# Kernel optimization log

Hardware: AMD Instinct MI355X
Metric: run time of the kernel (lower is better)

Reference implementation:

```python
import jax, jax.numpy as jnp
import numpy as np

B, D, L = 32, 64, 8192
K = 512
COMMITMENT_COST = 0.1


def setup_inputs() -> dict:
    key = jax.random.key(0)
    k1, k2 = jax.random.split(key)
    x = jax.random.normal(k1, (B, D, L), dtype=jnp.float32)
    # Embedding initialized uniform(-1/K, 1/K) as in the torch module
    weight = jax.random.uniform(k2, (K, D), dtype=jnp.float32, minval=-1.0 / K, maxval=1.0 / K)
    return {"x": x, "weight": weight}


def reference(x, weight):
    # x: [B, D, L] -> inputs: [B, L, D]
    inputs = jnp.transpose(x, (0, 2, 1))
    flat = inputs.reshape(-1, D)  # [N, D]
    # Squared L2 distances to codebook: [N, K]
    distances = (
        jnp.sum(flat * flat, axis=1, keepdims=True)
        + jnp.sum(weight * weight, axis=1)
        - 2.0 * flat @ weight.T
    )
    encoding_indices = jnp.argmin(distances, axis=1)  # [N]
    # Gather quantized vectors (equivalent to one-hot @ weight)
    quantized = weight[encoding_indices].reshape(inputs.shape)  # [B, L, D]
    e_latent_loss = jnp.mean((jax.lax.stop_gradient(quantized) - inputs) ** 2)
    q_latent_loss = jnp.mean((quantized - jax.lax.stop_gradient(inputs)) ** 2)
    loss = q_latent_loss + COMMITMENT_COST * e_latent_loss
    # Straight-through estimator
    quantized_st = inputs + jax.lax.stop_gradient(quantized - inputs)
    out = jnp.transpose(quantized_st, (0, 2, 1))  # [B, D, L]
    # perplexity = number of unique codes used (jit-friendly via bincount)
    perplexity = jnp.sum(jnp.bincount(encoding_indices, length=K) > 0)
    return (out, loss, perplexity, weight, encoding_indices[:, None])
```

## Files before the change

kernel.cpp:

```cpp
#include <hip/hip_runtime.h>
#include <math.h>

#define BB 32
#define DD 64
#define LL 8192
#define KK 512
#define NN (BB*LL)

#define OUT0_SZ  (BB*DD*LL)
#define LOSS_OFF (OUT0_SZ)
#define PERP_OFF (OUT0_SZ + 1)
#define W_OFF    (OUT0_SZ + 2)
#define IDX_OFF  (W_OFF + KK*DD)

#define WS_TVEC 0
#define WS_HIST 512
#define WS_LACC 1024
#define WS_WPH  1032
#define WS_WPL  (1032 + 16384)

typedef __attribute__((ext_vector_type(4))) float f32x4;
typedef __attribute__((ext_vector_type(8))) short s16x8;

#define WINDOW 1e-4f

__device__ __forceinline__ unsigned short f2bf(float f) {
  unsigned int u = __float_as_uint(f);
  return (unsigned short)((u + 0x7FFFu + ((u >> 16) & 1u)) >> 16);
}
__device__ __forceinline__ float bf2f(unsigned short s) {
  return __uint_as_float(((unsigned int)s) << 16);
}

__global__ void vq_init(const float* __restrict__ w, float* __restrict__ ws) {
#pragma clang fp contract(off)
  int t = blockIdx.x * blockDim.x + threadIdx.x;
  if (t < KK) {
    const float* wr = w + t * DD;
    float r[8];
#pragma unroll
    for (int j = 0; j < 8; j++) { float v = wr[j]; r[j] = v * v; }
#pragma unroll
    for (int blk = 8; blk < 64; blk += 8) {
#pragma unroll
      for (int j = 0; j < 8; j++) { float v = wr[blk + j]; float a = v * v; r[j] = r[j] + a; }
    }
    ws[WS_TVEC + t] = ((r[0] + r[1]) + (r[2] + r[3])) + ((r[4] + r[5]) + (r[6] + r[7]));
    ((int*)ws)[WS_HIST + t] = 0;
  }
  if (t == 0) ws[WS_LACC] = 0.0f;

  int j    = t & 7;
  int lane = (t >> 3) & 63;
  int ks   = (t >> 9) & 1;
  int ct   = t >> 10;
  int code = ct * 16 + (lane & 15);
  int d    = ks * 32 + ((lane >> 4) << 3) + j;
  float v  = w[code * DD + d];
  unsigned short h = f2bf(v);
  unsigned short l = f2bf(v - bf2f(h));
  ((unsigned short*)(ws + WS_WPH))[((ct * 2 + ks) * 64 + lane) * 8 + j] = h;
  ((unsigned short*)(ws + WS_WPL))[((ct * 2 + ks) * 64 + lane) * 8 + j] = l;
}

__launch_bounds__(256, 2)
__global__ void vq_main(const float* __restrict__ x, const float* __restrict__ w,
                        const float* __restrict__ ws, float* __restrict__ dout) {
#pragma clang fp contract(off)
  __shared__ unsigned short xstage[256 * 64];
  __shared__ float t_lds[KK];
  __shared__ float s_lds[256];
  __shared__ int   ccnt[256];
  __shared__ unsigned short cand[256][8];
  __shared__ unsigned char flags[KK];

  const float* tvec = ws + WS_TVEC;
  const s16x8* wph8 = (const s16x8*)(ws + WS_WPH);
  const s16x8* wpl8 = (const s16x8*)(ws + WS_WPL);
  int* hist = (int*)ws + WS_HIST;
  float* lacc = (float*)ws + WS_LACC;

  const int tid  = threadIdx.x;
  const int lane = tid & 63;
  const int wv   = tid >> 6;

  for (int e = tid; e < KK; e += 256) { t_lds[e] = tvec[e]; flags[e] = 0; }
  ccnt[tid] = 0;

  const int n = blockIdx.x * 256 + tid;
  const int b = n >> 13, l = n & 8191;
  const float* px = x + (size_t)b * DD * LL + l;

  float xr[64];
#pragma unroll
  for (int i = 0; i < 64; i++) xr[i] = px[(size_t)i * LL];

  float s;
  {
    float r[8];
#pragma unroll
    for (int j = 0; j < 8; j++) r[j] = xr[j] * xr[j];
#pragma unroll
    for (int blk = 8; blk < 64; blk += 8) {
#pragma unroll
      for (int j = 0; j < 8; j++) { float a = xr[blk + j] * xr[blk + j]; r[j] = r[j] + a; }
    }
    s = ((r[0] + r[1]) + (r[2] + r[3])) + ((r[4] + r[5]) + (r[6] + r[7]));
  }
  s_lds[tid] = s;

  {
    unsigned int* xs32 = (unsigned int*)xstage;
#pragma unroll
    for (int j = 0; j < 32; j++) {
      unsigned int v = (unsigned int)f2bf(xr[2 * j]) | ((unsigned int)f2bf(xr[2 * j + 1]) << 16);
      xs32[tid * 32 + j] = v;
    }
  }
  __syncthreads();

  s16x8 afh[4][2], afl[4][2];
  {
    const s16x8* xs8 = (const s16x8*)xstage;
#pragma unroll
    for (int tl = 0; tl < 4; tl++)
#pragma unroll
      for (int ks = 0; ks < 2; ks++)
        afh[tl][ks] = xs8[(wv * 64 + tl * 16 + (lane & 15)) * 8 + ks * 4 + (lane >> 4)];
  }
  __syncthreads();

  {
    unsigned int* xs32 = (unsigned int*)xstage;
#pragma unroll
    for (int j = 0; j < 32; j++) {
      float v0 = xr[2 * j],     h0 = bf2f(f2bf(v0));
      float v1 = xr[2 * j + 1], h1 = bf2f(f2bf(v1));
      unsigned int v = (unsigned int)f2bf(v0 - h0) | ((unsigned int)f2bf(v1 - h1) << 16);
      xs32[tid * 32 + j] = v;
    }
  }
  __syncthreads();
  {
    const s16x8* xs8 = (const s16x8*)xstage;
#pragma unroll
    for (int tl = 0; tl < 4; tl++)
#pragma unroll
      for (int ks = 0; ks < 2; ks++)
        afl[tl][ks] = xs8[(wv * 64 + tl * 16 + (lane & 15)) * 8 + ks * 4 + (lane >> 4)];
  }

  float sfr[4][4];
#pragma unroll
  for (int tl = 0; tl < 4; tl++)
#pragma unroll
    for (int r = 0; r < 4; r++)
      sfr[tl][r] = s_lds[wv * 64 + tl * 16 + ((lane >> 4) << 2) + r];

  unsigned long long t1[4][4], t2[4][4];
#pragma unroll
  for (int tl = 0; tl < 4; tl++)
#pragma unroll
    for (int r = 0; r < 4; r++) { t1[tl][r] = ~0ULL; t2[tl][r] = ~0ULL; }

#pragma clang loop unroll(disable)
  for (int ct = 0; ct < 32; ct++) {
    s16x8 bh0 = wph8[(ct * 2 + 0) * 64 + lane];
    s16x8 bh1 = wph8[(ct * 2 + 1) * 64 + lane];
    s16x8 bl0 = wpl8[(ct * 2 + 0) * 64 + lane];
    s16x8 bl1 = wpl8[(ct * 2 + 1) * 64 + lane];
    float tc = t_lds[ct * 16 + (lane & 15)];
    unsigned long long klo = (unsigned long long)(ct * 16 + (lane & 15));

#pragma unroll
    for (int tl = 0; tl < 4; tl++) {
      f32x4 acc = {0.f, 0.f, 0.f, 0.f};
      acc = __builtin_amdgcn_mfma_f32_16x16x32_bf16(afl[tl][0], bh0, acc, 0, 0, 0);
      acc = __builtin_amdgcn_mfma_f32_16x16x32_bf16(afl[tl][1], bh1, acc, 0, 0, 0);
      acc = __builtin_amdgcn_mfma_f32_16x16x32_bf16(afh[tl][0], bl0, acc, 0, 0, 0);
      acc = __builtin_amdgcn_mfma_f32_16x16x32_bf16(afh[tl][1], bl1, acc, 0, 0, 0);
      acc = __builtin_amdgcn_mfma_f32_16x16x32_bf16(afh[tl][0], bh0, acc, 0, 0, 0);
      acc = __builtin_amdgcn_mfma_f32_16x16x32_bf16(afh[tl][1], bh1, acc, 0, 0, 0);
#pragma unroll
      for (int r = 0; r < 4; r++) {
        float dap = fmaf(-2.0f, acc[r], sfr[tl][r] + tc);
        unsigned long long pk = (((unsigned long long)__float_as_uint(dap)) << 32) | klo;
        bool c1 = pk < t1[tl][r];
        bool c2 = pk < t2[tl][r];
        t2[tl][r] = c1 ? t1[tl][r] : (c2 ? pk : t2[tl][r]);
        t1[tl][r] = c1 ? pk : t1[tl][r];
      }
    }
  }

  unsigned long long g[4][4];
#pragma unroll
  for (int tl = 0; tl < 4; tl++)
#pragma unroll
    for (int r = 0; r < 4; r++) g[tl][r] = t1[tl][r];
#pragma unroll
  for (int m = 1; m <= 8; m <<= 1) {
#pragma unroll
    for (int tl = 0; tl < 4; tl++)
#pragma unroll
      for (int r = 0; r < 4; r++) {
        unsigned long long q = __shfl_xor(g[tl][r], m);
        g[tl][r] = q < g[tl][r] ? q : g[tl][r];
      }
  }

#pragma unroll
  for (int tl = 0; tl < 4; tl++)
#pragma unroll
    for (int r = 0; r < 4; r++) {
      int row = wv * 64 + tl * 16 + ((lane >> 4) << 2) + r;
      float thr = __uint_as_float((unsigned int)(g[tl][r] >> 32)) + WINDOW;
      float m1 = __uint_as_float((unsigned int)(t1[tl][r] >> 32));
      float m2 = __uint_as_float((unsigned int)(t2[tl][r] >> 32));
      bool in1 = (m1 <= thr), in2 = (m2 <= thr);
      if (in1) { int p = atomicAdd(&ccnt[row], 1); if (p < 8) cand[row][p] = (unsigned short)(t1[tl][r] & 0xFFFFu); }
      if (in2) { int p = atomicAdd(&ccnt[row], 1); if (p < 8) cand[row][p] = (unsigned short)(t2[tl][r] & 0xFFFFu); }
      if (in1 && in2) { int p = atomicAdd(&ccnt[row], 1); if (p < 8) cand[row][p] = (unsigned short)(512 + (lane & 15)); }
    }
  __syncthreads();

  int kwin;
  {
    int cnt = ccnt[tid];
    if (cnt == 1) {
      kwin = cand[tid][0];
    } else {
      unsigned long long best = ~0ULL;
      auto evalExact = [&](int c) {
        const float4* wr = (const float4*)(w + c * DD);
        float gg = 0.0f;
#pragma unroll
        for (int i = 0; i < 16; i++) {
          float4 wq = wr[i];
          gg = fmaf(xr[4 * i + 0], wq.x, gg); gg = fmaf(xr[4 * i + 1], wq.y, gg);
          gg = fmaf(xr[4 * i + 2], wq.z, gg); gg = fmaf(xr[4 * i + 3], wq.w, gg);
        }
        float de = fmaf(-2.0f, gg, s + t_lds[c]);
        unsigned long long pk = (((unsigned long long)__float_as_uint(de)) << 32) | (unsigned long long)c;
        if (pk < best) best = pk;
      };
      if (cnt > 8) {
        for (int c = 0; c < KK; c++) evalExact(c);
      } else {
        for (int i = 0; i < cnt; i++) {
          int c = cand[tid][i];
          if (c < 512) evalExact(c);
          else { int c0 = c - 512; for (int jj = 0; jj < 32; jj++) evalExact(jj * 16 + c0); }
        }
      }
      kwin = (int)(best & 0xFFFFu);
    }
  }

  float ls = 0.0f;
  {
    float* o = dout + (size_t)b * DD * LL + l;
    const float4* wr = (const float4*)(w + kwin * DD);
#pragma unroll
    for (int i = 0; i < 16; i++) {
      float4 v = wr[i];
      o[(size_t)(4 * i + 0) * LL] = v.x; o[(size_t)(4 * i + 1) * LL] = v.y;
      o[(size_t)(4 * i + 2) * LL] = v.z; o[(size_t)(4 * i + 3) * LL] = v.w;
      float df;
      df = v.x - xr[4 * i + 0]; ls = fmaf(df, df, ls);
      df = v.y - xr[4 * i + 1]; ls = fmaf(df, df, ls);
      df = v.z - xr[4 * i + 2]; ls = fmaf(df, df, ls);
      df = v.w - xr[4 * i + 3]; ls = fmaf(df, df, ls);
    }
  }
  dout[IDX_OFF + n] = (float)kwin;

#pragma unroll
  for (int o = 32; o > 0; o >>= 1) ls += __shfl_down(ls, o);
  if ((tid & 63) == 0) atomicAdd(lacc, ls);

  flags[kwin] = 1;
  __syncthreads();
  for (int e = tid; e < KK; e += 256)
    if (flags[e]) atomicOr(&hist[e], 1);
}

__global__ void vq_final(const float* __restrict__ w, const float* __restrict__ ws,
                         float* __restrict__ dout) {
  __shared__ int red[512];
  const int* hist = (const int*)ws + WS_HIST;
  int tid = threadIdx.x;
  red[tid] = (hist[tid] != 0) ? 1 : 0;
  __syncthreads();
  for (int sx = 256; sx > 0; sx >>= 1) {
    if (tid < sx) red[tid] += red[tid + sx];
    __syncthreads();
  }
  if (tid == 0) {
    dout[PERP_OFF] = (float)red[0];
    float m = ws[WS_LACC] / 16777216.0f;
    dout[LOSS_OFF] = m + 0.1f * m;
  }
  const float2* w2 = (const float2*)w;
  float2* o2 = (float2*)(dout + W_OFF);
  for (int j = tid; j < KK * DD / 2; j += 512) o2[j] = w2[j];
}

extern "C" void kernel_launch(void* const* d_in, const int* in_sizes, int n_in,
                              void* d_out, int out_size, void* d_ws, size_t ws_size,
                              hipStream_t stream) {
  const float* x = (const float*)d_in[0];
  const float* w = (const float*)d_in[1];
  float* dout = (float*)d_out;
  float* ws = (float*)d_ws;

  vq_init<<<128, 256, 0, stream>>>(w, ws);
  vq_main<<<NN / 256, 256, 0, stream>>>(x, w, ws, dout);
  vq_final<<<1, 512, 0, stream>>>(w, ws, dout);
}
```

Before: 246.0 us.

## Split each row across two lanes, swizzle LDS staging, prefetch codebook tiles

Each input row is now handled by two lanes, each loading half of the 64 features. This halves register pressure and doubles the grid size, at the cost of more MFMA passes per codebook tile relative to rows. The LDS staging for the bf16 hi/lo split uses XOR swizzling to avoid bank conflicts. Codebook fragments for the next tile are prefetched in the loop, and the top-2 tracking uses float plus a tile index instead of packed 64-bit keys. The weight copy moves from the single-block final kernel into the init kernel. The exact re-check now reloads the upper half of x from global memory and keeps only 4 candidate slots.

```diff
diff --git a/kernel.cpp b/kernel.cpp
--- a/kernel.cpp
+++ b/kernel.cpp
@@ -21,6 +21,7 @@
 
 typedef __attribute__((ext_vector_type(4))) float f32x4;
 typedef __attribute__((ext_vector_type(8))) short s16x8;
+typedef unsigned long long u64;
 
 #define WINDOW 1e-4f
 
@@ -31,8 +32,14 @@
 __device__ __forceinline__ float bf2f(unsigned short s) {
   return __uint_as_float(((unsigned int)s) << 16);
 }
-
-__global__ void vq_init(const float* __restrict__ w, float* __restrict__ ws) {
+__device__ __forceinline__ u64 shflx64(u64 v, int m) {
+  unsigned lo = __shfl_xor((unsigned)v, m);
+  unsigned hi = __shfl_xor((unsigned)(v >> 32), m);
+  return ((u64)hi << 32) | lo;
+}
+
+__global__ void vq_init(const float* __restrict__ w, float* __restrict__ ws,
+                        float* __restrict__ dout) {
 #pragma clang fp contract(off)
   int t = blockIdx.x * blockDim.x + threadIdx.x;
   if (t < KK) {
@@ -50,28 +57,35 @@
   }
   if (t == 0) ws[WS_LACC] = 0.0f;
 
-  int j    = t & 7;
-  int lane = (t >> 3) & 63;
-  int ks   = (t >> 9) & 1;
-  int ct   = t >> 10;
-  int code = ct * 16 + (lane & 15);
-  int d    = ks * 32 + ((lane >> 4) << 3) + j;
-  float v  = w[code * DD + d];
-  unsigned short h = f2bf(v);
-  unsigned short l = f2bf(v - bf2f(h));
-  ((unsigned short*)(ws + WS_WPH))[((ct * 2 + ks) * 64 + lane) * 8 + j] = h;
-  ((unsigned short*)(ws + WS_WPL))[((ct * 2 + ks) * 64 + lane) * 8 + j] = l;
+  {
+    int j    = t & 7;
+    int lane = (t >> 3) & 63;
+    int ks   = (t >> 9) & 1;
+    int ct   = t >> 10;
+    int code = ct * 16 + (lane & 15);
+    int d    = ks * 32 + ((lane >> 4) << 3) + j;
+    float v  = w[code * DD + d];
+    unsigned short h = f2bf(v);
+    unsigned short l = f2bf(v - bf2f(h));
+    ((unsigned short*)(ws + WS_WPH))[((ct * 2 + ks) * 64 + lane) * 8 + j] = h;
+    ((unsigned short*)(ws + WS_WPL))[((ct * 2 + ks) * 64 + lane) * 8 + j] = l;
+  }
+
+  if (t < KK * DD / 2) {
+    ((float2*)(dout + W_OFF))[t] = ((const float2*)w)[t];
+  }
 }
 
 __launch_bounds__(256, 2)
 __global__ void vq_main(const float* __restrict__ x, const float* __restrict__ w,
                         const float* __restrict__ ws, float* __restrict__ dout) {
 #pragma clang fp contract(off)
-  __shared__ unsigned short xstage[256 * 64];
+  __shared__ uint4 xstage[4][32][8];
   __shared__ float t_lds[KK];
-  __shared__ float s_lds[256];
-  __shared__ int   ccnt[256];
-  __shared__ unsigned short cand[256][8];
+  __shared__ float s_lds[128];
+  __shared__ u64   g_lds[128];
+  __shared__ unsigned short cand[128][4];
+  __shared__ int   ccnt[128];
   __shared__ unsigned char flags[KK];
 
   const float* tvec = ws + WS_TVEC;
@@ -83,210 +97,249 @@
   const int tid  = threadIdx.x;
   const int lane = tid & 63;
   const int wv   = tid >> 6;
+  const int rloc = lane & 31;
+  const int half = lane >> 5;
+  const int res  = lane & 15;
 
   for (int e = tid; e < KK; e += 256) { t_lds[e] = tvec[e]; flags[e] = 0; }
-  ccnt[tid] = 0;
-
-  const int n = blockIdx.x * 256 + tid;
+  if (tid < 128) ccnt[tid] = 0;
+
+  const int n = blockIdx.x * 128 + wv * 32 + rloc;
   const int b = n >> 13, l = n & 8191;
   const float* px = x + (size_t)b * DD * LL + l;
 
-  float xr[64];
-#pragma unroll
-  for (int i = 0; i < 64; i++) xr[i] = px[(size_t)i * LL];
-
-  float s;
+  float xh[32];
+#pragma unroll
+  for (int i = 0; i < 32; i++) xh[i] = px[(size_t)(half * 32 + i) * LL];
+
+  float s_apx;
   {
     float r[8];
 #pragma unroll
-    for (int j = 0; j < 8; j++) r[j] = xr[j] * xr[j];
-#pragma unroll
-    for (int blk = 8; blk < 64; blk += 8) {
-#pragma unroll
-      for (int j = 0; j < 8; j++) { float a = xr[blk + j] * xr[blk + j]; r[j] = r[j] + a; }
-    }
-    s = ((r[0] + r[1]) + (r[2] + r[3])) + ((r[4] + r[5]) + (r[6] + r[7]));
-  }
-  s_lds[tid] = s;
-
+    for (int j = 0; j < 8; j++) r[j] = xh[j] * xh[j];
+#pragma unroll
+    for (int blk = 8; blk < 32; blk += 8) {
+#pragma unroll
+      for (int j = 0; j < 8; j++) { float a = xh[blk + j] * xh[blk + j]; r[j] = r[j] + a; }
+    }
+    float sh = ((r[0] + r[1]) + (r[2] + r[3])) + ((r[4] + r[5]) + (r[6] + r[7]));
+    float so = __shfl(sh, lane ^ 32);
+    float slo = half ? so : sh, shi = half ? sh : so;
+    s_apx = slo + shi;
+    if (half == 0) s_lds[wv * 32 + rloc] = s_apx;
+  }
+
+  uint4* xs4 = (uint4*)xstage;
+  const s16x8* xs8 = (const s16x8*)xstage;
+  s16x8 afh[2][2], afl[2][2];
   {
-    unsigned int* xs32 = (unsigned int*)xstage;
-#pragma unroll
-    for (int j = 0; j < 32; j++) {
-      unsigned int v = (unsigned int)f2bf(xr[2 * j]) | ((unsigned int)f2bf(xr[2 * j + 1]) << 16);
-      xs32[tid * 32 + j] = v;
-    }
-  }
-  __syncthreads();
-
-  s16x8 afh[4][2], afl[4][2];
-  {
-    const s16x8* xs8 = (const s16x8*)xstage;
-#pragma unroll
-    for (int tl = 0; tl < 4; tl++)
-#pragma unroll
-      for (int ks = 0; ks < 2; ks++)
-        afh[tl][ks] = xs8[(wv * 64 + tl * 16 + (lane & 15)) * 8 + ks * 4 + (lane >> 4)];
-  }
-  __syncthreads();
-
-  {
-    unsigned int* xs32 = (unsigned int*)xstage;
-#pragma unroll
-    for (int j = 0; j < 32; j++) {
-      float v0 = xr[2 * j],     h0 = bf2f(f2bf(v0));
-      float v1 = xr[2 * j + 1], h1 = bf2f(f2bf(v1));
-      unsigned int v = (unsigned int)f2bf(v0 - h0) | ((unsigned int)f2bf(v1 - h1) << 16);
-      xs32[tid * 32 + j] = v;
-    }
-  }
-  __syncthreads();
-  {
-    const s16x8* xs8 = (const s16x8*)xstage;
-#pragma unroll
-    for (int tl = 0; tl < 4; tl++)
-#pragma unroll
-      for (int ks = 0; ks < 2; ks++)
-        afl[tl][ks] = xs8[(wv * 64 + tl * 16 + (lane & 15)) * 8 + ks * 4 + (lane >> 4)];
-  }
-
-  float sfr[4][4];
-#pragma unroll
-  for (int tl = 0; tl < 4; tl++)
+    unsigned int pk[16];
+#pragma unroll
+    for (int m = 0; m < 16; m++)
+      pk[m] = (unsigned int)f2bf(xh[2 * m]) | ((unsigned int)f2bf(xh[2 * m + 1]) << 16);
+#pragma unroll
+    for (int q = 0; q < 4; q++) {
+      int sw = (half * 4 + q) ^ (rloc & 7);
+      uint4 v; v.x = pk[4 * q]; v.y = pk[4 * q + 1]; v.z = pk[4 * q + 2]; v.w = pk[4 * q + 3];
+      xs4[(wv * 32 + rloc) * 8 + sw] = v;
+    }
+    __syncthreads();
+#pragma unroll
+    for (int t2 = 0; t2 < 2; t2++)
+#pragma unroll
+      for (int ks = 0; ks < 2; ks++) {
+        int row = t2 * 16 + (lane & 15);
+        int sw = (ks * 4 + (lane >> 4)) ^ (lane & 7);
+        afh[t2][ks] = xs8[(wv * 32 + row) * 8 + sw];
+      }
+    __syncthreads();
+#pragma unroll
+    for (int m = 0; m < 16; m++) {
+      float v0 = xh[2 * m],     h0 = bf2f(f2bf(v0));
+      float v1 = xh[2 * m + 1], h1 = bf2f(f2bf(v1));
+      pk[m] = (unsigned int)f2bf(v0 - h0) | ((unsigned int)f2bf(v1 - h1) << 16);
+    }
+#pragma unroll
+    for (int q = 0; q < 4; q++) {
+      int sw = (half * 4 + q) ^ (rloc & 7);
+      uint4 v; v.x = pk[4 * q]; v.y = pk[4 * q + 1]; v.z = pk[4 * q + 2]; v.w = pk[4 * q + 3];
+      xs4[(wv * 32 + rloc) * 8 + sw] = v;
+    }
+    __syncthreads();
+#pragma unroll
+    for (int t2 = 0; t2 < 2; t2++)
+#pragma unroll
+      for (int ks = 0; ks < 2; ks++) {
+        int row = t2 * 16 + (lane & 15);
+        int sw = (ks * 4 + (lane >> 4)) ^ (lane & 7);
+        afl[t2][ks] = xs8[(wv * 32 + row) * 8 + sw];
+      }
+  }
+
+  float sfr[2][4];
+#pragma unroll
+  for (int t2 = 0; t2 < 2; t2++)
 #pragma unroll
     for (int r = 0; r < 4; r++)
-      sfr[tl][r] = s_lds[wv * 64 + tl * 16 + ((lane >> 4) << 2) + r];
-
-  unsigned long long t1[4][4], t2[4][4];
-#pragma unroll
-  for (int tl = 0; tl < 4; tl++)
-#pragma unroll
-    for (int r = 0; r < 4; r++) { t1[tl][r] = ~0ULL; t2[tl][r] = ~0ULL; }
+      sfr[t2][r] = s_lds[wv * 32 + t2 * 16 + ((lane >> 4) << 2) + r];
+
+  float d1[2][4], d2[2][4]; int k1[2][4];
+#pragma unroll
+  for (int t2 = 0; t2 < 2; t2++)
+#pragma unroll
+    for (int r = 0; r < 4; r++) { d1[t2][r] = INFINITY; d2[t2][r] = INFINITY; k1[t2][r] = 0; }
+
+  s16x8 bh0 = wph8[lane], bh1 = wph8[64 + lane];
+  s16x8 bl0 = wpl8[lane], bl1 = wpl8[64 + lane];
+  float tc = t_lds[res];
 
 #pragma clang loop unroll(disable)
   for (int ct = 0; ct < 32; ct++) {
-    s16x8 bh0 = wph8[(ct * 2 + 0) * 64 + lane];
-    s16x8 bh1 = wph8[(ct * 2 + 1) * 64 + lane];
-    s16x8 bl0 = wpl8[(ct * 2 + 0) * 64 + lane];
-    s16x8 bl1 = wpl8[(ct * 2 + 1) * 64 + lane];
-    float tc = t_lds[ct * 16 + (lane & 15)];
-    unsigned long long klo = (unsigned long long)(ct * 16 + (lane & 15));
-
-#pragma unroll
-    for (int tl = 0; tl < 4; tl++) {
+    int cn = (ct + 1) & 31;
+    s16x8 nh0 = wph8[cn * 128 + lane],      nh1 = wph8[cn * 128 + 64 + lane];
+    s16x8 nl0 = wpl8[cn * 128 + lane],      nl1 = wpl8[cn * 128 + 64 + lane];
+    float ntc = t_lds[cn * 16 + res];
+
+#pragma unroll
+    for (int t2 = 0; t2 < 2; t2++) {
       f32x4 acc = {0.f, 0.f, 0.f, 0.f};
-      acc = __builtin_amdgcn_mfma_f32_16x16x32_bf16(afl[tl][0], bh0, acc, 0, 0, 0);
-      acc = __builtin_amdgcn_mfma_f32_16x16x32_bf16(afl[tl][1], bh1, acc, 0, 0, 0);
-      acc = __builtin_amdgcn_mfma_f32_16x16x32_bf16(afh[tl][0], bl0, acc, 0, 0, 0);
-      acc = __builtin_amdgcn_mfma_f32_16x16x32_bf16(afh[tl][1], bl1, acc, 0, 0, 0);
-      acc = __builtin_amdgcn_mfma_f32_16x16x32_bf16(afh[tl][0], bh0, acc, 0, 0, 0);
-      acc = __builtin_amdgcn_mfma_f32_16x16x32_bf16(afh[tl][1], bh1, acc, 0, 0, 0);
+      acc = __builtin_amdgcn_mfma_f32_16x16x32_bf16(afl[t2][0], bh0, acc, 0, 0, 0);
+      acc = __builtin_amdgcn_mfma_f32_16x16x32_bf16(afl[t2][1], bh1, acc, 0, 0, 0);
+      acc = __builtin_amdgcn_mfma_f32_16x16x32_bf16(afh[t2][0], bl0, acc, 0, 0, 0);
+      acc = __builtin_amdgcn_mfma_f32_16x16x32_bf16(afh[t2][1], bl1, acc, 0, 0, 0);
+      acc = __builtin_amdgcn_mfma_f32_16x16x32_bf16(afh[t2][0], bh0, acc, 0, 0, 0);
+      acc = __builtin_amdgcn_mfma_f32_16x16x32_bf16(afh[t2][1], bh1, acc, 0, 0, 0);
 #pragma unroll
       for (int r = 0; r < 4; r++) {
-        float dap = fmaf(-2.0f, acc[r], sfr[tl][r] + tc);
-        unsigned long long pk = (((unsigned long long)__float_as_uint(dap)) << 32) | klo;
-        bool c1 = pk < t1[tl][r];
-        bool c2 = pk < t2[tl][r];
-        t2[tl][r] = c1 ? t1[tl][r] : (c2 ? pk : t2[tl][r]);
-        t1[tl][r] = c1 ? pk : t1[tl][r];
-      }
-    }
-  }
-
-  unsigned long long g[4][4];
-#pragma unroll
-  for (int tl = 0; tl < 4; tl++)
-#pragma unroll
-    for (int r = 0; r < 4; r++) g[tl][r] = t1[tl][r];
-#pragma unroll
-  for (int m = 1; m <= 8; m <<= 1) {
-#pragma unroll
-    for (int tl = 0; tl < 4; tl++)
-#pragma unroll
-      for (int r = 0; r < 4; r++) {
-        unsigned long long q = __shfl_xor(g[tl][r], m);
-        g[tl][r] = q < g[tl][r] ? q : g[tl][r];
-      }
-  }
-
-#pragma unroll
-  for (int tl = 0; tl < 4; tl++)
+        float u = sfr[t2][r] + tc;
+        float dap = fmaf(-2.0f, acc[r], u);
+        bool c1 = dap < d1[t2][r];
+        bool c2 = dap < d2[t2][r];
+        d2[t2][r] = c1 ? d1[t2][r] : (c2 ? dap : d2[t2][r]);
+        d1[t2][r] = c1 ? dap : d1[t2][r];
+        k1[t2][r] = c1 ? ct : k1[t2][r];
+      }
+    }
+    bh0 = nh0; bh1 = nh1; bl0 = nl0; bl1 = nl1; tc = ntc;
+  }
+
+  u64 gmin[2][4];
+#pragma unroll
+  for (int t2 = 0; t2 < 2; t2++)
 #pragma unroll
     for (int r = 0; r < 4; r++) {
-      int row = wv * 64 + tl * 16 + ((lane >> 4) << 2) + r;
-      float thr = __uint_as_float((unsigned int)(g[tl][r] >> 32)) + WINDOW;
-      float m1 = __uint_as_float((unsigned int)(t1[tl][r] >> 32));
-      float m2 = __uint_as_float((unsigned int)(t2[tl][r] >> 32));
-      bool in1 = (m1 <= thr), in2 = (m2 <= thr);
-      if (in1) { int p = atomicAdd(&ccnt[row], 1); if (p < 8) cand[row][p] = (unsigned short)(t1[tl][r] & 0xFFFFu); }
-      if (in2) { int p = atomicAdd(&ccnt[row], 1); if (p < 8) cand[row][p] = (unsigned short)(t2[tl][r] & 0xFFFFu); }
-      if (in1 && in2) { int p = atomicAdd(&ccnt[row], 1); if (p < 8) cand[row][p] = (unsigned short)(512 + (lane & 15)); }
+      u64 pk = (((u64)__float_as_uint(d1[t2][r])) << 32) | (u64)(k1[t2][r] * 16 + res);
+      u64 q1 = shflx64(pk, 1); pk = pk < q1 ? pk : q1;
+      u64 q2 = shflx64(pk, 2); pk = pk < q2 ? pk : q2;
+      u64 q4 = shflx64(pk, 4); pk = pk < q4 ? pk : q4;
+      u64 q8 = shflx64(pk, 8); pk = pk < q8 ? pk : q8;
+      gmin[t2][r] = pk;
+    }
+
+#pragma unroll
+  for (int t2 = 0; t2 < 2; t2++)
+#pragma unroll
+    for (int r = 0; r < 4; r++) {
+      int row = wv * 32 + t2 * 16 + ((lane >> 4) << 2) + r;
+      if (res == 0) g_lds[row] = gmin[t2][r];
+      float thr = __uint_as_float((unsigned)(gmin[t2][r] >> 32)) + WINDOW;
+      bool in1 = d1[t2][r] <= thr;
+      bool in2 = d2[t2][r] <= thr;
+      if (in1) { int p = atomicAdd(&ccnt[row], 1); if (p < 4) cand[row][p] = (unsigned short)(k1[t2][r] * 16 + res); }
+      if (in2) { int p = atomicAdd(&ccnt[row], 1); if (p < 4) cand[row][p] = (unsigned short)(512 + res); }
     }
   __syncthreads();
 
-  int kwin;
-  {
-    int cnt = ccnt[tid];
-    if (cnt == 1) {
-      kwin = cand[tid][0];
+  int kwin = 0;
+  if (lane < 32) {
+    int row = wv * 32 + lane;
+    int cnt = ccnt[row];
+    if (cnt <= 1) {
+      kwin = (int)(g_lds[row] & 0x1FFu);
     } else {
-      unsigned long long best = ~0ULL;
+      float xu[32];
+#pragma unroll
+      for (int i = 0; i < 32; i++) xu[i] = px[(size_t)(32 + i) * LL];
+      float s;
+      {
+        float r[8];
+#pragma unroll
+        for (int j = 0; j < 8; j++) r[j] = xh[j] * xh[j];
+#pragma unroll
+        for (int blk = 8; blk < 32; blk += 8)
+#pragma unroll
+          for (int j = 0; j < 8; j++) { float a = xh[blk + j] * xh[blk + j]; r[j] = r[j] + a; }
+#pragma unroll
+        for (int blk = 0; blk < 32; blk += 8)
+#pragma unroll
+          for (int j = 0; j < 8; j++) { float a = xu[blk + j] * xu[blk + j]; r[j] = r[j] + a; }
+        s = ((r[0] + r[1]) + (r[2] + r[3])) + ((r[4] + r[5]) + (r[6] + r[7]));
+      }
+      u64 best = ~0ULL;
       auto evalExact = [&](int c) {
         const float4* wr = (const float4*)(w + c * DD);
         float gg = 0.0f;
 #pragma unroll
-        for (int i = 0; i < 16; i++) {
+        for (int i = 0; i < 8; i++) {
           float4 wq = wr[i];
-          gg = fmaf(xr[4 * i + 0], wq.x, gg); gg = fmaf(xr[4 * i + 1], wq.y, gg);
-          gg = fmaf(xr[4 * i + 2], wq.z, gg); gg = fmaf(xr[4 * i + 3], wq.w, gg);
+          gg = fmaf(xh[4 * i + 0], wq.x, gg); gg = fmaf(xh[4 * i + 1], wq.y, gg);
+          gg = fmaf(xh[4 * i + 2], wq.z, gg); gg = fmaf(xh[4 * i + 3], wq.w, gg);
+        }
+#pragma unroll
+        for (int i = 0; i < 8; i++) {
+          float4 wq = wr[8 + i];
+          gg = fmaf(xu[4 * i + 0], wq.x, gg); gg = fmaf(xu[4 * i + 1], wq.y, gg);
+          gg = fmaf(xu[4 * i + 2], wq.z, gg); gg = fmaf(xu[4 * i + 3], wq.w, gg);
         }
         float de = fmaf(-2.0f, gg, s + t_lds[c]);
-        unsigned long long pk = (((unsigned long long)__float_as_uint(de)) << 32) | (unsigned long long)c;
+        u64 pk = (((u64)__float_as_uint(de)) << 32) | (u64)c;
         if (pk < best) best = pk;
       };
-      if (cnt > 8) {
+      if (cnt > 4) {
         for (int c = 0; c < KK; c++) evalExact(c);
       } else {
         for (int i = 0; i < cnt; i++) {
-          int c = cand[tid][i];
+          int c = cand[row][i];
           if (c < 512) evalExact(c);
           else { int c0 = c - 512; for (int jj = 0; jj < 32; jj++) evalExact(jj * 16 + c0); }
         }
       }
-      kwin = (int)(best & 0xFFFFu);
-    }
-  }
+      kwin = (int)(best & 0x1FFu);
+    }
+  }
+  kwin = __shfl(kwin, lane & 31);
 
   float ls = 0.0f;
   {
-    float* o = dout + (size_t)b * DD * LL + l;
-    const float4* wr = (const float4*)(w + kwin * DD);
-#pragma unroll
-    for (int i = 0; i < 16; i++) {
+    const float4* wr = (const float4*)(w + kwin * DD) + half * 8;
+    float* o = dout + (size_t)b * DD * LL + l + (size_t)half * 32 * LL;
+#pragma unroll
+    for (int i = 0; i < 8; i++) {
       float4 v = wr[i];
       o[(size_t)(4 * i + 0) * LL] = v.x; o[(size_t)(4 * i + 1) * LL] = v.y;
       o[(size_t)(4 * i + 2) * LL] = v.z; o[(size_t)(4 * i + 3) * LL] = v.w;
       float df;
-      df = v.x - xr[4 * i + 0]; ls = fmaf(df, df, ls);
-      df = v.y - xr[4 * i + 1]; ls = fmaf(df, df, ls);
-      df = v.z - xr[4 * i + 2]; ls = fmaf(df, df, ls);
-      df = v.w - xr[4 * i + 3]; ls = fmaf(df, df, ls);
-    }
-  }
-  dout[IDX_OFF + n] = (float)kwin;
+      df = v.x - xh[4 * i + 0]; ls = fmaf(df, df, ls);
+      df = v.y - xh[4 * i + 1]; ls = fmaf(df, df, ls);
+      df = v.z - xh[4 * i + 2]; ls = fmaf(df, df, ls);
+      df = v.w - xh[4 * i + 3]; ls = fmaf(df, df, ls);
+    }
+  }
+  if (half == 0) {
+    dout[IDX_OFF + n] = (float)kwin;
+    flags[kwin] = 1;
+  }
 
 #pragma unroll
   for (int o = 32; o > 0; o >>= 1) ls += __shfl_down(ls, o);
   if ((tid & 63) == 0) atomicAdd(lacc, ls);
 
-  flags[kwin] = 1;
   __syncthreads();
   for (int e = tid; e < KK; e += 256)
     if (flags[e]) atomicOr(&hist[e], 1);
 }
 
-__global__ void vq_final(const float* __restrict__ w, const float* __restrict__ ws,
-                         float* __restrict__ dout) {
+__global__ void vq_final(const float* __restrict__ ws, float* __restrict__ dout) {
   __shared__ int red[512];
   const int* hist = (const int*)ws + WS_HIST;
   int tid = threadIdx.x;
@@ -301,9 +354,6 @@
     float m = ws[WS_LACC] / 16777216.0f;
     dout[LOSS_OFF] = m + 0.1f * m;
   }
-  const float2* w2 = (const float2*)w;
-  float2* o2 = (float2*)(dout + W_OFF);
-  for (int j = tid; j < KK * DD / 2; j += 512) o2[j] = w2[j];
 }
 
 extern "C" void kernel_launch(void* const* d_in, const int* in_sizes, int n_in,
@@ -314,7 +364,7 @@
   float* dout = (float*)d_out;
   float* ws = (float*)d_ws;
 
-  vq_init<<<128, 256, 0, stream>>>(w, ws);
-  vq_main<<<NN / 256, 256, 0, stream>>>(x, w, ws, dout);
-  vq_final<<<1, 512, 0, stream>>>(w, ws, dout);
-}
+  vq_init<<<128, 256, 0, stream>>>(w, ws, dout);
+  vq_main<<<NN / 128, 256, 0, stream>>>(x, w, ws, dout);
+  vq_final<<<1, 512, 0, stream>>>(ws, dout);
+}
```

Result: slower. 307.5 us (+25.0%).
